# Performance work log

Hardware: AMD Instinct MI355X
Metric: run time of the kernel (lower is better)

Reference implementation:

```python
import jax, jax.numpy as jnp
import numpy as np

N_HEADS = 12


def gconv1x1(x, w, b, groups):
    # x: [B, C, T, S]; w: [O, C//groups] (1x1 kernel squeezed); b: [O]
    B, C, T, S = x.shape
    O, I = w.shape
    xr = x.reshape(B, groups, C // groups, T, S)
    wr = w.reshape(groups, O // groups, I)
    y = jnp.einsum('bgits,goi->bgots', xr, wr).reshape(B, O, T, S)
    return y + b[None, :, None, None]


def setup_inputs() -> dict:
    key = jax.random.key(0)
    ks = jax.random.split(key, 16)
    B, T, E = 2, 512, 768
    H = N_HEADS
    s = 0.02
    inp = {
        'x': jax.random.normal(ks[0], (B, T, E), jnp.float32),
        # fc_q / fc_k / fc_v (torch Linear: y = x @ W.T + b)
        'wq': jax.random.normal(ks[1], (E, E), jnp.float32) * s,
        'bq': jax.random.normal(ks[2], (E,), jnp.float32) * s,
        'wk': jax.random.normal(ks[3], (E, E), jnp.float32) * s,
        'bk': jax.random.normal(ks[4], (E,), jnp.float32) * s,
        'wv': jax.random.normal(ks[5], (E, E), jnp.float32) * s,
        'bv': jax.random.normal(ks[6], (E,), jnp.float32) * s,
        # ConvolutionOp: all 1x1 grouped convs, groups=12
        # conv_inner_subspace_1: in=144 -> out=96  (w: [96, 12])
        'w1': jax.random.normal(ks[7], (8 * H, H), jnp.float32) * s,
        'b1': jax.random.normal(ks[8], (8 * H,), jnp.float32) * s,
        # conv_inner_subspace_2: in=96 -> out=12   (w: [12, 8])
        'w2': jax.random.normal(ks[9], (H, 8), jnp.float32) * s,
        'b2': jax.random.normal(ks[10], (H,), jnp.float32) * s,
        # conv_cross_subspace_1: in=12 -> out=48   (w: [48, 1])
        'w3': jax.random.normal(ks[11], (4 * H, 1), jnp.float32) * s,
        'b3': jax.random.normal(ks[12], (4 * H,), jnp.float32) * s,
        # conv_cross_subspace_2: in=48 -> out=12   (w: [12, 4])
        'w4': jax.random.normal(ks[13], (H, 4), jnp.float32) * s,
        'b4': jax.random.normal(ks[14], (H,), jnp.float32) * s,
    }
    return inp


def reference(x, wq, bq, wk, bk, wv, bv, w1, b1, w2, b2, w3, b3, w4, b4):
    B, T, E = x.shape
    H = N_HEADS
    hd = E // H
    scale = E ** 0.5  # note: sqrt(embed_dim), not sqrt(head_dim)

    def heads(y):  # [B,T,E] -> [H,B,T,hd]
        return y.reshape(B, T, H, hd).transpose(2, 0, 1, 3)

    q = heads(x @ wq.T + bq)
    k = heads(x @ wk.T + bk)
    v = heads(x @ wv.T + bv)

    # all head-pair QK^T: channel index = q_head * H + k_head (matches torch stack order)
    attn = jnp.einsum('qbld,kbtd->qkblt', q, k) / scale          # [H,H,B,T,T]
    attn = attn.transpose(2, 0, 1, 3, 4).reshape(B, H * H, T, T)  # [B,144,T,T]

    # talking-heads style grouped 1x1 conv mixing
    a = jax.nn.relu(gconv1x1(attn, w1, b1, H))   # [B,96,T,T]
    a = gconv1x1(a, w2, b2, H)                    # [B,12,T,T]
    a = jax.nn.relu(gconv1x1(a, w3, b3, H))      # [B,48,T,T]
    a = gconv1x1(a, w4, b4, H)                    # [B,12,T,T]

    # weighted V sum; rearrange 'head b t d -> b t (head d)'
    ctx = jnp.einsum('bhlt,hbtd->blhd', a, v).reshape(B, T, E)
    return ctx
```

## Files before the change

kernel.cpp:

```cpp
#include <hip/hip_runtime.h>

#define DEVINL __device__ __forceinline__

constexpr int E    = 768;
constexpr int TSEQ = 512;
constexpr int NH   = 12;
constexpr int HD   = 64;
constexpr float RSCALE = 0.036084391824351615f;

typedef short bf16x8 __attribute__((ext_vector_type(8)));
typedef float floatx4 __attribute__((ext_vector_type(4)));

DEVINL short f2bf(float x) {
    union { float f; unsigned u; } v; v.f = x;
    unsigned r = v.u + 0x7FFFu + ((v.u >> 16) & 1u);
    return (short)(r >> 16);
}
DEVINL float bf2f(short s) {
    union { unsigned u; float f; } v;
    v.u = ((unsigned)(unsigned short)s) << 16;
    return v.f;
}

__global__ __launch_bounds__(256) void convert_kernel(
    const float* __restrict__ x,  const float* __restrict__ wq,
    const float* __restrict__ wk, const float* __restrict__ wv,
    short* __restrict__ xb, short* __restrict__ wqb,
    short* __restrict__ wkb, short* __restrict__ wvb)
{
    const int g = blockIdx.x * 256 + threadIdx.x;
    const float* src; short* dst; int off;
    if (g < 98304)       { src = x;  dst = xb;  off = g * 8; }
    else if (g < 172032) { src = wq; dst = wqb; off = (g - 98304) * 8; }
    else if (g < 245760) { src = wk; dst = wkb; off = (g - 172032) * 8; }
    else                 { src = wv; dst = wvb; off = (g - 245760) * 8; }
    float4 f0 = *(const float4*)&src[off];
    float4 f1 = *(const float4*)&src[off + 4];
    bf16x8 o;
    o[0] = f2bf(f0.x); o[1] = f2bf(f0.y); o[2] = f2bf(f0.z); o[3] = f2bf(f0.w);
    o[4] = f2bf(f1.x); o[5] = f2bf(f1.y); o[6] = f2bf(f1.z); o[7] = f2bf(f1.w);
    *(bf16x8*)&dst[off] = o;
}

__global__ __launch_bounds__(256) void qkv_mfma(
    const short* __restrict__ xb,
    const short* __restrict__ wqb, const float* __restrict__ bq,
    const short* __restrict__ wkb, const float* __restrict__ bk,
    const short* __restrict__ wvb, const float* __restrict__ bv,
    short* __restrict__ Qo, short* __restrict__ Ko, short* __restrict__ Vo)
{
    const short* W; const float* bias; short* outp;
    if (blockIdx.z == 0)      { W = wqb; bias = bq; outp = Qo; }
    else if (blockIdx.z == 1) { W = wkb; bias = bk; outp = Ko; }
    else                      { W = wvb; bias = bv; outp = Vo; }

    __shared__ short As[64 * 72];
    __shared__ short Bs[64 * 72];

    const int m0   = blockIdx.x * 64;
    const int n0   = blockIdx.y * 64;
    const int tid  = threadIdx.x;
    const int wvi  = tid >> 6;
    const int lane = tid & 63;
    const int col  = lane & 15;
    const int quad = lane >> 4;

    const int r0 = tid >> 3,   kc0 = tid & 7;
    const int r1 = r0 + 32;

    floatx4 acc[4];
    #pragma unroll
    for (int i = 0; i < 4; i++) acc[i] = (floatx4){0.f, 0.f, 0.f, 0.f};

    for (int k0 = 0; k0 < E; k0 += 64) {
        bf16x8 a0 = *(const bf16x8*)&xb[(size_t)(m0 + r0) * E + k0 + kc0 * 8];
        bf16x8 a1 = *(const bf16x8*)&xb[(size_t)(m0 + r1) * E + k0 + kc0 * 8];
        bf16x8 b0 = *(const bf16x8*)&W [(size_t)(n0 + r0) * E + k0 + kc0 * 8];
        bf16x8 b1 = *(const bf16x8*)&W [(size_t)(n0 + r1) * E + k0 + kc0 * 8];
        __syncthreads();
        *(bf16x8*)&As[r0 * 72 + kc0 * 8] = a0;
        *(bf16x8*)&As[r1 * 72 + kc0 * 8] = a1;
        *(bf16x8*)&Bs[r0 * 72 + kc0 * 8] = b0;
        *(bf16x8*)&Bs[r1 * 72 + kc0 * 8] = b1;
        __syncthreads();
        #pragma unroll
        for (int k32 = 0; k32 < 2; k32++) {
            bf16x8 bf = *(const bf16x8*)&Bs[(wvi*16 + col) * 72 + k32*32 + quad*8];
            #pragma unroll
            for (int ms = 0; ms < 4; ms++) {
                bf16x8 af = *(const bf16x8*)&As[(ms*16 + col) * 72 + k32*32 + quad*8];
                acc[ms] = __builtin_amdgcn_mfma_f32_16x16x32_bf16(af, bf, acc[ms], 0, 0, 0);
            }
        }
    }

    const float bn = bias[n0 + wvi*16 + col];
    const int h = blockIdx.y;
    #pragma unroll
    for (int ms = 0; ms < 4; ms++) {
        #pragma unroll
        for (int r = 0; r < 4; r++) {
            int m = m0 + ms*16 + quad*4 + r;
            int bb = m >> 9, l = m & 511;
            outp[(((size_t)(bb*NH + h)) * TSEQ + l) * HD + wvi*16 + col] =
                f2bf(acc[ms][r] + bn);
        }
    }
}

__global__ __launch_bounds__(256) void kmix_kernel(
    const short* __restrict__ K,
    const float* __restrict__ w1,
    short* __restrict__ Kp)
{
    const int g  = blockIdx.x * 256 + threadIdx.x;
    const int d8 = g & 7;
    const int t  = (g >> 3) & 511;
    const int o  = (g >> 12) & 7;
    const int bh = g >> 15;
    const int h  = bh % NH;
    const int b  = bh / NH;

    float acc[8] = {};
    #pragma unroll
    for (int i = 0; i < 12; i++) {
        float w = w1[(h*8 + o)*12 + i] * RSCALE;
        bf16x8 kv = *(const bf16x8*)&K[(((size_t)(b*NH + i) * TSEQ) + t) * HD + d8*8];
        #pragma unroll
        for (int j = 0; j < 8; j++)
            acc[j] = fmaf(w, bf2f(kv[j]), acc[j]);
    }
    bf16x8 outv;
    #pragma unroll
    for (int j = 0; j < 8; j++) outv[j] = f2bf(acc[j]);
    *(bf16x8*)&Kp[(size_t)g * 8] = outv;
}

DEVINL float mlp_eval(const float s[8],
                      const float b1r[8], const float w2r[8], float b2r,
                      const float w3r[4], const float b3r[4],
                      const float w4r[4], float b4r)
{
    float z2 = b2r;
    #pragma unroll
    for (int o = 0; o < 8; o++) {
        float z1 = fmaxf(s[o] + b1r[o], 0.0f);
        z2 = fmaf(z1, w2r[o], z2);
    }
    float r = b4r;
    #pragma unroll
    for (int j = 0; j < 4; j++) {
        float z3 = fmaxf(fmaf(z2, w3r[j], b3r[j]), 0.0f);
        r = fmaf(z3, w4r[j], r);
    }
    return r;
}

DEVINL int vrow(int r) { return r*40 + (r >> 3)*8; }

__global__ __launch_bounds__(256, 3) void attn_mfma(
    const short* __restrict__ Qg,
    const short* __restrict__ Kg,
    const short* __restrict__ Vg,
    const float* __restrict__ b1, const float* __restrict__ w2,
    const float* __restrict__ b2, const float* __restrict__ w3,
    const float* __restrict__ b3, const float* __restrict__ w4,
    const float* __restrict__ b4,
    float* __restrict__ Pout)
{
    __shared__ short Ks[256 * 72];
    __shared__ short Vt[2624];
    __shared__ short As[2624];

    const int blk = blockIdx.x;
    const int qtr = blk & 3;
    const int lt  = (blk >> 2) & 7;
    const int bh  = blk >> 5;
    const int h   = bh % NH;
    const int l0  = lt * 64;
    const int tb  = qtr * 128;

    const int tid  = threadIdx.x;
    const int wv   = tid >> 6;
    const int lane = tid & 63;
    const int col  = lane & 15;
    const int quad = lane >> 4;
    const int wl   = wv >> 1;
    const int wt   = wv & 1;

    float b1r[8], w2r[8], w3r[4], b3r[4], w4r[4];
    #pragma unroll
    for (int o = 0; o < 8; o++) { b1r[o] = b1[h*8+o]; w2r[o] = w2[h*8+o]; }
    #pragma unroll
    for (int j = 0; j < 4; j++) { w3r[j] = w3[h*4+j]; b3r[j] = b3[h*4+j]; w4r[j] = w4[h*4+j]; }
    const float b2r = b2[h];
    const float b4r = b4[h];

    bf16x8 qa[2][2];
    {
        const short* qb = Qg + ((size_t)bh * TSEQ + l0 + wl*32 + col) * HD;
        qa[0][0] = *(const bf16x8*)&qb[quad*8];
        qa[0][1] = *(const bf16x8*)&qb[32 + quad*8];
        qa[1][0] = *(const bf16x8*)&qb[16*HD + quad*8];
        qa[1][1] = *(const bf16x8*)&qb[16*HD + 32 + quad*8];
    }

    floatx4 accO[4];
    #pragma unroll
    for (int d16 = 0; d16 < 4; d16++) accO[d16] = (floatx4){0.f, 0.f, 0.f, 0.f};

    const short* kbase = Kg + (size_t)bh * 8 * TSEQ * HD;
    const short* vbase = Vg + (size_t)bh * TSEQ * HD;

    const int tl = tid >> 3;
    const int dc = tid & 7;

    for (int it = 0; it < 4; it++) {
        const int t0 = tb + it * 32;

        bf16x8 ktmp[8];
        #pragma unroll
        for (int o = 0; o < 8; o++)
            ktmp[o] = *(const bf16x8*)&kbase[((size_t)o * TSEQ + t0 + tl) * HD + dc*8];
        bf16x8 vtmp = *(const bf16x8*)&vbase[(size_t)(t0 + tl) * HD + dc*8];

        __syncthreads();

        #pragma unroll
        for (int o = 0; o < 8; o++)
            *(bf16x8*)&Ks[(o*32 + tl)*72 + dc*8] = ktmp[o];
        #pragma unroll
        for (int j = 0; j < 8; j++)
            Vt[vrow(dc*8 + j) + tl] = vtmp[j];

        __syncthreads();

        floatx4 accS[8][2];
        #pragma unroll
        for (int o = 0; o < 8; o++) {
            accS[o][0] = (floatx4){0.f, 0.f, 0.f, 0.f};
            accS[o][1] = (floatx4){0.f, 0.f, 0.f, 0.f};
        }
        #pragma unroll
        for (int k32 = 0; k32 < 2; k32++) {
            #pragma unroll
            for (int o = 0; o < 8; o++) {
                bf16x8 bf = *(const bf16x8*)&Ks[(o*32 + wt*16 + col)*72 + k32*32 + quad*8];
                accS[o][0] = __builtin_amdgcn_mfma_f32_16x16x32_bf16(qa[0][k32], bf, accS[o][0], 0, 0, 0);
                accS[o][1] = __builtin_amdgcn_mfma_f32_16x16x32_bf16(qa[1][k32], bf, accS[o][1], 0, 0, 0);
            }
        }

        #pragma unroll
        for (int li = 0; li < 2; li++) {
            #pragma unroll
            for (int r = 0; r < 4; r++) {
                float s[8];
                #pragma unroll
                for (int o = 0; o < 8; o++) s[o] = accS[o][li][r];
                float a = mlp_eval(s, b1r, w2r, b2r, w3r, b3r, w4r, b4r);
                As[vrow(wl*32 + li*16 + quad*4 + r) + wt*16 + col] = f2bf(a);
            }
        }
        __syncthreads();

        bf16x8 af = *(const bf16x8*)&As[vrow(wv*16 + col) + quad*8];
        #pragma unroll
        for (int d16 = 0; d16 < 4; d16++) {
            bf16x8 vf = *(const bf16x8*)&Vt[vrow(d16*16 + col) + quad*8];
            accO[d16] = __builtin_amdgcn_mfma_f32_16x16x32_bf16(af, vf, accO[d16], 0, 0, 0);
        }
    }

    float* pb = Pout + (size_t)blk * 64 * 64;
    #pragma unroll
    for (int d16 = 0; d16 < 4; d16++)
        #pragma unroll
        for (int r = 0; r < 4; r++)
            pb[(wv*16 + quad*4 + r) * 64 + d16*16 + col] = accO[d16][r];
}

__global__ __launch_bounds__(256) void reduce_kernel(
    const float* __restrict__ P, float* __restrict__ out)
{
    const int gi  = blockIdx.x * 256 + threadIdx.x;
    const int d4  = gi & 15;
    const int r   = (gi >> 4) & 63;
    const int grp = gi >> 10;
    const int lt  = grp & 7;
    const int bh  = grp >> 3;
    const int h   = bh % NH;
    const int b   = bh / NH;

    const float* p0 = P + (size_t)grp * 4 * 4096 + r * 64 + d4 * 4;
    float4 s0 = *(const float4*)&p0[0];
    float4 s1 = *(const float4*)&p0[4096];
    float4 s2 = *(const float4*)&p0[8192];
    float4 s3 = *(const float4*)&p0[12288];
    float4 s;
    s.x = (s0.x + s1.x) + (s2.x + s3.x);
    s.y = (s0.y + s1.y) + (s2.y + s3.y);
    s.z = (s0.z + s1.z) + (s2.z + s3.z);
    s.w = (s0.w + s1.w) + (s2.w + s3.w);
    *(float4*)&out[((size_t)(b*TSEQ + lt*64 + r)) * E + h*64 + d4*4] = s;
}

extern "C" void kernel_launch(void* const* d_in, const int* in_sizes, int n_in,
                              void* d_out, int out_size, void* d_ws, size_t ws_size,
                              hipStream_t stream) {
    const float* x  = (const float*)d_in[0];
    const float* wq = (const float*)d_in[1];
    const float* bq = (const float*)d_in[2];
    const float* wk = (const float*)d_in[3];
    const float* bk = (const float*)d_in[4];
    const float* wv = (const float*)d_in[5];
    const float* bv = (const float*)d_in[6];
    const float* w1 = (const float*)d_in[7];
    const float* b1 = (const float*)d_in[8];
    const float* w2 = (const float*)d_in[9];
    const float* b2 = (const float*)d_in[10];
    const float* w3 = (const float*)d_in[11];
    const float* b3 = (const float*)d_in[12];
    const float* w4 = (const float*)d_in[13];
    const float* b4 = (const float*)d_in[14];
    float* out = (float*)d_out;

    short* Qb = (short*)d_ws;
    short* Kb = Qb + 786432;
    short* Vb = Kb + 786432;
    short* Kp = Vb + 786432;
    float* P  = (float*)(Kp + 6291456);
    short* xb  = (short*)P;
    short* wqb = xb + 786432;
    short* wkb = wqb + 589824;
    short* wvb = wkb + 589824;

    convert_kernel<<<1248, 256, 0, stream>>>(x, wq, wk, wv, xb, wqb, wkb, wvb);
    qkv_mfma<<<dim3(16, 12, 3), 256, 0, stream>>>(xb, wqb, bq, wkb, bk, wvb, bv, Qb, Kb, Vb);
    kmix_kernel<<<3072, 256, 0, stream>>>(Kb, w1, Kp);
    attn_mfma<<<768, 256, 0, stream>>>(Qb, Kp, Vb, b1, w2, b2, w3, b3, w4, b4, P);
    reduce_kernel<<<768, 256, 0, stream>>>(P, out);
}
```

Before: 132.1 us.

## Fuse fp32-to-bf16 conversion into QKV GEMM and prefetch next tiles in registers

Removes the separate conversion kernel and has the QKV GEMM read fp32 x and weights directly, converting to bf16 while loading tiles. Both the QKV GEMM and the attention kernel now issue the global loads for the next K/V tile right after the shared-memory stores, so load latency overlaps with the MFMA work on the current tile. This saves one launch and a round trip through the bf16 workspace, but the GEMM re-reads fp32 data (twice the bytes) across blocks and keeps more registers live for the prefetch buffers.

```diff
diff --git a/kernel.cpp b/kernel.cpp
--- a/kernel.cpp
+++ b/kernel.cpp
@@ -22,37 +22,26 @@
     return v.f;
 }
 
-__global__ __launch_bounds__(256) void convert_kernel(
-    const float* __restrict__ x,  const float* __restrict__ wq,
-    const float* __restrict__ wk, const float* __restrict__ wv,
-    short* __restrict__ xb, short* __restrict__ wqb,
-    short* __restrict__ wkb, short* __restrict__ wvb)
-{
-    const int g = blockIdx.x * 256 + threadIdx.x;
-    const float* src; short* dst; int off;
-    if (g < 98304)       { src = x;  dst = xb;  off = g * 8; }
-    else if (g < 172032) { src = wq; dst = wqb; off = (g - 98304) * 8; }
-    else if (g < 245760) { src = wk; dst = wkb; off = (g - 172032) * 8; }
-    else                 { src = wv; dst = wvb; off = (g - 245760) * 8; }
-    float4 f0 = *(const float4*)&src[off];
-    float4 f1 = *(const float4*)&src[off + 4];
+DEVINL bf16x8 cvt8(const float* p) {
+    float4 f0 = *(const float4*)p;
+    float4 f1 = *(const float4*)(p + 4);
     bf16x8 o;
     o[0] = f2bf(f0.x); o[1] = f2bf(f0.y); o[2] = f2bf(f0.z); o[3] = f2bf(f0.w);
     o[4] = f2bf(f1.x); o[5] = f2bf(f1.y); o[6] = f2bf(f1.z); o[7] = f2bf(f1.w);
-    *(bf16x8*)&dst[off] = o;
+    return o;
 }
 
 __global__ __launch_bounds__(256) void qkv_mfma(
-    const short* __restrict__ xb,
-    const short* __restrict__ wqb, const float* __restrict__ bq,
-    const short* __restrict__ wkb, const float* __restrict__ bk,
-    const short* __restrict__ wvb, const float* __restrict__ bv,
+    const float* __restrict__ x,
+    const float* __restrict__ wq, const float* __restrict__ bq,
+    const float* __restrict__ wk, const float* __restrict__ bk,
+    const float* __restrict__ wv, const float* __restrict__ bv,
     short* __restrict__ Qo, short* __restrict__ Ko, short* __restrict__ Vo)
 {
-    const short* W; const float* bias; short* outp;
-    if (blockIdx.z == 0)      { W = wqb; bias = bq; outp = Qo; }
-    else if (blockIdx.z == 1) { W = wkb; bias = bk; outp = Ko; }
-    else                      { W = wvb; bias = bv; outp = Vo; }
+    const float* W; const float* bias; short* outp;
+    if (blockIdx.z == 0)      { W = wq; bias = bq; outp = Qo; }
+    else if (blockIdx.z == 1) { W = wk; bias = bk; outp = Ko; }
+    else                      { W = wv; bias = bv; outp = Vo; }
 
     __shared__ short As[64 * 72];
     __shared__ short Bs[64 * 72];
@@ -72,17 +61,26 @@
     #pragma unroll
     for (int i = 0; i < 4; i++) acc[i] = (floatx4){0.f, 0.f, 0.f, 0.f};
 
+    bf16x8 a0 = cvt8(&x[(size_t)(m0 + r0) * E + kc0 * 8]);
+    bf16x8 a1 = cvt8(&x[(size_t)(m0 + r1) * E + kc0 * 8]);
+    bf16x8 b0 = cvt8(&W[(size_t)(n0 + r0) * E + kc0 * 8]);
+    bf16x8 b1 = cvt8(&W[(size_t)(n0 + r1) * E + kc0 * 8]);
+
     for (int k0 = 0; k0 < E; k0 += 64) {
-        bf16x8 a0 = *(const bf16x8*)&xb[(size_t)(m0 + r0) * E + k0 + kc0 * 8];
-        bf16x8 a1 = *(const bf16x8*)&xb[(size_t)(m0 + r1) * E + k0 + kc0 * 8];
-        bf16x8 b0 = *(const bf16x8*)&W [(size_t)(n0 + r0) * E + k0 + kc0 * 8];
-        bf16x8 b1 = *(const bf16x8*)&W [(size_t)(n0 + r1) * E + k0 + kc0 * 8];
         __syncthreads();
         *(bf16x8*)&As[r0 * 72 + kc0 * 8] = a0;
         *(bf16x8*)&As[r1 * 72 + kc0 * 8] = a1;
         *(bf16x8*)&Bs[r0 * 72 + kc0 * 8] = b0;
         *(bf16x8*)&Bs[r1 * 72 + kc0 * 8] = b1;
         __syncthreads();
+
+        if (k0 + 64 < E) {
+            a0 = cvt8(&x[(size_t)(m0 + r0) * E + k0 + 64 + kc0 * 8]);
+            a1 = cvt8(&x[(size_t)(m0 + r1) * E + k0 + 64 + kc0 * 8]);
+            b0 = cvt8(&W[(size_t)(n0 + r0) * E + k0 + 64 + kc0 * 8]);
+            b1 = cvt8(&W[(size_t)(n0 + r1) * E + k0 + 64 + kc0 * 8]);
+        }
+
         #pragma unroll
         for (int k32 = 0; k32 < 2; k32++) {
             bf16x8 bf = *(const bf16x8*)&Bs[(wvi*16 + col) * 72 + k32*32 + quad*8];
@@ -215,15 +213,13 @@
     const int tl = tid >> 3;
     const int dc = tid & 7;
 
+    bf16x8 ktmp[8]; bf16x8 vtmp;
+    #pragma unroll
+    for (int o = 0; o < 8; o++)
+        ktmp[o] = *(const bf16x8*)&kbase[((size_t)o * TSEQ + tb + tl) * HD + dc*8];
+    vtmp = *(const bf16x8*)&vbase[(size_t)(tb + tl) * HD + dc*8];
+
     for (int it = 0; it < 4; it++) {
-        const int t0 = tb + it * 32;
-
-        bf16x8 ktmp[8];
-        #pragma unroll
-        for (int o = 0; o < 8; o++)
-            ktmp[o] = *(const bf16x8*)&kbase[((size_t)o * TSEQ + t0 + tl) * HD + dc*8];
-        bf16x8 vtmp = *(const bf16x8*)&vbase[(size_t)(t0 + tl) * HD + dc*8];
-
         __syncthreads();
 
         #pragma unroll
@@ -234,6 +230,14 @@
             Vt[vrow(dc*8 + j) + tl] = vtmp[j];
 
         __syncthreads();
+
+        if (it < 3) {
+            const int t1 = tb + (it + 1) * 32;
+            #pragma unroll
+            for (int o = 0; o < 8; o++)
+                ktmp[o] = *(const bf16x8*)&kbase[((size_t)o * TSEQ + t1 + tl) * HD + dc*8];
+            vtmp = *(const bf16x8*)&vbase[(size_t)(t1 + tl) * HD + dc*8];
+        }
 
         floatx4 accS[8][2];
         #pragma unroll
@@ -330,13 +334,8 @@
     short* Vb = Kb + 786432;
     short* Kp = Vb + 786432;
     float* P  = (float*)(Kp + 6291456);
-    short* xb  = (short*)P;
-    short* wqb = xb + 786432;
-    short* wkb = wqb + 589824;
-    short* wvb = wkb + 589824;
-
-    convert_kernel<<<1248, 256, 0, stream>>>(x, wq, wk, wv, xb, wqb, wkb, wvb);
-    qkv_mfma<<<dim3(16, 12, 3), 256, 0, stream>>>(xb, wqb, bq, wkb, bk, wvb, bv, Qb, Kb, Vb);
+
+    qkv_mfma<<<dim3(16, 12, 3), 256, 0, stream>>>(x, wq, bq, wk, bk, wv, bv, Qb, Kb, Vb);
     kmix_kernel<<<3072, 256, 0, stream>>>(Kb, w1, Kp);
     attn_mfma<<<768, 256, 0, stream>>>(Qb, Kp, Vb, b1, w2, b2, w3, b3, w4, b4, P);
     reduce_kernel<<<768, 256, 0, stream>>>(P, out);
```

After: 145.3 us. 10.0% more time.
